# Kernel optimization log

Measured on AMD Instinct MI355X. Metric: run time of the kernel, lower is better.

The kernel has to match this reference:

```python
import jax, jax.numpy as jnp
import numpy as np

B, C, H, W = 4, 128, 256, 256
N_KPTS = 2048
N_POS = 8
KS = 3
CH = 2 * N_POS  # channel_num (mask=False)


def setup_inputs() -> dict:
    key = jax.random.key(0)
    ks = jax.random.split(key, 8)
    x = jax.random.normal(ks[0], (B, C, H, W), jnp.float32)
    keypoints = jax.random.uniform(ks[1], (B, N_KPTS, 2), jnp.float32, -1.0, 1.0)
    s1 = 1.0 / np.sqrt(C * KS * KS)
    W1 = jax.random.uniform(ks[2], (CH, C, KS, KS), jnp.float32, -s1, s1)
    b1 = jax.random.uniform(ks[3], (CH,), jnp.float32, -s1, s1)
    s2 = 1.0 / np.sqrt(CH)
    W2 = jax.random.uniform(ks[4], (CH, CH), jnp.float32, -s2, s2)
    b2 = jax.random.uniform(ks[5], (CH,), jnp.float32, -s2, s2)
    s3 = 1.0 / np.sqrt(C)
    sf_w = jax.random.uniform(ks[6], (C, C), jnp.float32, -s3, s3)
    agg_w = jax.random.uniform(ks[7], (N_POS, C, C), jnp.float32)  # torch.rand
    return {"x": x, "keypoints": keypoints, "W1": W1, "b1": b1,
            "W2": W2, "b2": b2, "sf_w": sf_w, "agg_w": agg_w}


def _bilinear(img, px, py):
    """grid_sample(bilinear, align_corners=True, padding=zeros) in pixel coords.
    img: [c,h,w]; px,py: [M] -> [c,M]."""
    h, w = img.shape[1], img.shape[2]
    x0f = jnp.floor(px); y0f = jnp.floor(py)
    x0 = x0f.astype(jnp.int32); y0 = y0f.astype(jnp.int32)
    wx1 = px - x0f; wy1 = py - y0f
    wx0 = 1.0 - wx1; wy0 = 1.0 - wy1

    def tap(yi, xi, wgt):
        valid = (xi >= 0) & (xi < w) & (yi >= 0) & (yi < h)
        v = img[:, jnp.clip(yi, 0, h - 1), jnp.clip(xi, 0, w - 1)]
        return v * (wgt * valid)[None]

    return (tap(y0, x0, wy0 * wx0) + tap(y0, x0 + 1, wy0 * wx1)
            + tap(y0 + 1, x0, wy1 * wx0) + tap(y0 + 1, x0 + 1, wy1 * wx1))


def reference(x, keypoints, W1, b1, W2, b2, sf_w, agg_w):
    wh = jnp.array([W - 1, H - 1], jnp.float32)
    max_off = max(H, W) / 4.0
    taps = jnp.arange(KS)

    def per_image(xi, kpts):
        kwh = (kpts / 2.0 + 0.5) * wh                     # [N,2] pixel coords (x,y)
        rc = kwh.astype(jnp.int32)                        # .long() trunc (coords >= 0)
        # corner = trunc(rc - ps/2 + 1) then clamp -> rc-1 clamped (ps=3)
        lim = jnp.array([W - 1 - KS, H - 1 - KS])
        corner = jnp.clip(rc - 1, 0, lim)                 # [N,2] (x,y)
        rows = corner[:, 1, None] + taps                  # [N,ks]
        cols = corner[:, 0, None] + taps                  # [N,ks]
        patch = xi[:, rows[:, :, None], cols[:, None, :]] # [c,N,ks,ks]
        patch = patch.transpose(1, 0, 2, 3)               # [N,c,ks,ks]
        # offset_conv: 3x3 conv (valid, ->1x1) + ReLU + 1x1 conv
        h1 = jax.nn.relu(jnp.einsum('ncab,ocab->no', patch, W1) + b1)
        off = h1 @ W2.T + b2                              # [N,2*n_pos]
        off = jnp.clip(off, -max_off, max_off)
        offset = off.reshape(-1, 2, N_POS).transpose(0, 2, 1)  # [N,n_pos,2]
        pos = kwh[:, None, :] + offset                    # [N,n_pos,2] pixel coords
        # 2*pos/wh - 1 then align_corners unnormalize == pos
        feat = _bilinear(xi, pos[..., 0].reshape(-1), pos[..., 1].reshape(-1))  # [c,N*p]
        feat = feat.reshape(C, -1, N_POS).transpose(1, 0, 2)  # [N,c,p]
        feat = jax.nn.selu(jnp.einsum('oc,ncp->nop', sf_w, feat))
        descs = jnp.einsum('ncp,pcd->nd', feat, agg_w)    # [N,dims]
        nrm = jnp.maximum(jnp.linalg.norm(descs, axis=1, keepdims=True), 1e-12)
        return descs / nrm, offset

    descriptors, offsets = jax.vmap(per_image)(x, keypoints)
    return descriptors, offsets
```

## Files before the change

kernel.cpp:

```cpp
#include <hip/hip_runtime.h>
#include <hip/hip_bf16.h>
#include <math.h>

#define B_ 4
#define C_ 128
#define H_ 256
#define W_ 256
#define NK 2048
#define NP 8
#define HW_ (H_*W_)
#define MAXOFF 64.0f
#define NROWS (B_*NK)

typedef short s16x8 __attribute__((ext_vector_type(8)));
typedef short s16x4 __attribute__((ext_vector_type(4)));
typedef float f32x4 __attribute__((ext_vector_type(4)));

#define SELU_SC 1.0507009873554805f
#define SELU_AL 1.6732632423543772f

#define N_W1F (36*64*8)
#define N_SFB (8*4*64*8)
#define N_AGG (8*8*4*64*8)

__device__ inline float bf2f(short b) {
    union { unsigned int u; float f; } cv;
    cv.u = ((unsigned int)(unsigned short)b) << 16;
    return cv.f;
}
__device__ inline short f2bf_s(float f) {
    __hip_bfloat16 h = __float2bfloat16(f);
    return *(short*)&h;
}

__global__ __launch_bounds__(256) void k_transpose_bf(const float* __restrict__ x,
                                                      __hip_bfloat16* __restrict__ xt) {
    __shared__ float tile[32][33];
    int bid = blockIdx.x;
    int xb = bid & 7;  bid >>= 3;
    int cb = bid & 3;  bid >>= 2;
    int y  = bid & 255; bid >>= 8;
    int i  = bid;
    int tx  = threadIdx.x & 31;
    int ty0 = threadIdx.x >> 5;
    const float* src = x + ((size_t)(i*C_ + cb*32)*H_ + y)*W_ + xb*32;
    #pragma unroll
    for (int k = 0; k < 4; ++k) {
        int c = ty0 + k*8;
        tile[c][tx] = src[(size_t)c*HW_ + tx];
    }
    __syncthreads();
    int tx2 = threadIdx.x & 15;
    int xo8 = threadIdx.x >> 4;
    __hip_bfloat16* dst = xt + ((size_t)(i*H_ + y)*W_ + xb*32)*C_ + cb*32;
    #pragma unroll
    for (int k = 0; k < 2; ++k) {
        int xo = xo8 + k*16;
        __hip_bfloat162 v;
        v.x = __float2bfloat16(tile[tx2*2][xo]);
        v.y = __float2bfloat16(tile[tx2*2+1][xo]);
        *(__hip_bfloat162*)(dst + (size_t)xo*C_ + tx2*2) = v;
    }
}

__global__ __launch_bounds__(256) void k_prep_all(const float* __restrict__ W1,
        const float* __restrict__ sf_w, const float* __restrict__ agg_w,
        __hip_bfloat16* __restrict__ w1f, __hip_bfloat16* __restrict__ sfb,
        __hip_bfloat16* __restrict__ aggb) {
    int t = blockIdx.x*256 + threadIdx.x;
    if (t < N_W1F) {
        int e = t & 7, l = (t >> 3) & 63, ks = t >> 9;
        int o = l & 15, c = (ks & 3)*32 + ((l >> 4) << 3) + e, ab = ks >> 2;
        w1f[t] = __float2bfloat16(W1[o*1152 + c*9 + ab]);
    } else if (t < N_W1F + N_SFB) {
        int u = t - N_W1F;
        int e = u & 7, l = (u >> 3) & 63, ks = (u >> 9) & 3, j = u >> 11;
        sfb[u] = __float2bfloat16(sf_w[(j*16 + (l & 15))*128 + ks*32 + ((l >> 4) << 3) + e]);
    } else if (t < N_W1F + N_SFB + N_AGG) {
        int u = t - N_W1F - N_SFB;
        int e = u & 7, l = (u >> 3) & 63, ks = (u >> 9) & 3, p = (u >> 11) & 7, jd = u >> 14;
        aggb[u] = __float2bfloat16(agg_w[((size_t)p*128 + ks*32 + ((l >> 4) << 3) + e)*128 + jd*16 + (l & 15)]);
    }
}

#define FSTR 1032
#define HSTR 136
#define RSTR 132
__global__ __launch_bounds__(256) void k_fused(
        const __hip_bfloat16* __restrict__ xtb, const float* __restrict__ kpts,
        const __hip_bfloat16* __restrict__ w1f, const float* __restrict__ b1,
        const float* __restrict__ W2, const float* __restrict__ b2,
        const __hip_bfloat16* __restrict__ sfb, const __hip_bfloat16* __restrict__ aggb,
        float* __restrict__ out_off, float* __restrict__ descs) {
    __shared__ __align__(16) char reg0[33792];
    __shared__ __align__(16) char reg1[17408];
    __shared__ float Cp[4][16][17];
    __shared__ float hL[16][17];
    __shared__ float W2s[16][16];
    __shared__ float posL[16][8][2];
    __shared__ float kwx[16], kwy[16];
    __shared__ int   kcx[16], kcy[16];

    int t = threadIdx.x;
    int blk = blockIdx.x;
    int i = blk >> 7;
    int w = t >> 6, l = t & 63;
    int r16 = l & 15, q = l >> 4;
    int kp0 = blk * 16;

    if (t < 16) {
        int gk = kp0 + t;
        float kx = kpts[(size_t)gk*2], ky = kpts[(size_t)gk*2 + 1];
        float wx = (kx*0.5f + 0.5f) * (float)(W_-1);
        float wy = (ky*0.5f + 0.5f) * (float)(H_-1);
        int cx = (int)wx - 1; cx = min(max(cx, 0), W_-1-3);
        int cy = (int)wy - 1; cy = min(max(cy, 0), H_-1-3);
        kwx[t] = wx; kwy[t] = wy; kcx[t] = cx; kcy[t] = cy;
    }
    W2s[t >> 4][t & 15] = W2[t];
    __syncthreads();

    {
        const char* pb = (const char*)(xtb +
            ((size_t)(i*H_ + kcy[r16])*W_ + kcx[r16])*C_);
        f32x4 acc = {0.f, 0.f, 0.f, 0.f};
        #pragma unroll
        for (int s = 0; s < 9; ++s) {
            int ks = w*9 + s;
            int ab = ks >> 2;
            int a = ab/3, b = ab - (ab/3)*3;
            int off = ((a*W_ + b)*C_ + (ks & 3)*32 + q*8) * 2;
            s16x8 af = *(const s16x8*)(pb + off);
            s16x8 bf = *(const s16x8*)((const short*)w1f + ((size_t)ks*64 + l)*8);
            acc = __builtin_amdgcn_mfma_f32_16x16x32_bf16(af, bf, acc, 0, 0, 0);
        }
        #pragma unroll
        for (int r = 0; r < 4; ++r)
            Cp[w][q*4 + r][r16] = acc[r];
    }
    __syncthreads();
    {
        int kp = t >> 4, o = t & 15;
        float sum = Cp[0][kp][o] + Cp[1][kp][o] + Cp[2][kp][o] + Cp[3][kp][o];
        hL[kp][o] = fmaxf(sum + b1[o], 0.f);
        __syncthreads();
        float acc2 = b2[o];
        #pragma unroll
        for (int oo = 0; oo < 16; ++oo)
            acc2 += hL[kp][oo] * W2s[o][oo];
        acc2 = fminf(fmaxf(acc2, -MAXOFF), MAXOFF);
        int d = o >> 3, p = o & 7;
        int gk = kp0 + kp;
        out_off[((size_t)gk*NP + p)*2 + d] = acc2;
        posL[kp][p][d] = (d ? kwy[kp] : kwx[kp]) + acc2;
    }
    __syncthreads();

    __hip_bfloat16* featL = (__hip_bfloat16*)reg0;
    {
        int half = t >> 5, lane32 = t & 31;
        int c0 = lane32 * 4;
        #pragma unroll 4
        for (int s = 0; s < 16; ++s) {
            int pr = s*8 + half;
            int kp = pr >> 3, p = pr & 7;
            float px = posL[kp][p][0], py = posL[kp][p][1];
            float x0f = floorf(px), y0f = floorf(py);
            int x0 = (int)x0f, y0 = (int)y0f;
            float wx1 = px - x0f, wy1 = py - y0f;
            float wx0 = 1.f - wx1, wy0 = 1.f - wy1;
            float a0 = 0.f, a1 = 0.f, a2 = 0.f, a3 = 0.f;
            #pragma unroll
            for (int tap = 0; tap < 4; ++tap) {
                int xi = x0 + (tap & 1);
                int yi = y0 + (tap >> 1);
                float wgt = ((tap & 1) ? wx1 : wx0) * ((tap >> 1) ? wy1 : wy0);
                bool valid = (xi >= 0) & (xi < W_) & (yi >= 0) & (yi < H_);
                int xc = min(max(xi, 0), W_-1);
                int yc = min(max(yi, 0), H_-1);
                float wv = valid ? wgt : 0.f;
                const __hip_bfloat16* src = xtb + ((size_t)(i*H_ + yc)*W_ + xc)*C_ + c0;
                s16x4 v = *(const s16x4*)src;
                a0 += wv * bf2f(v[0]);
                a1 += wv * bf2f(v[1]);
                a2 += wv * bf2f(v[2]);
                a3 += wv * bf2f(v[3]);
            }
            s16x4 ov;
            ov[0] = f2bf_s(a0); ov[1] = f2bf_s(a1);
            ov[2] = f2bf_s(a2); ov[3] = f2bf_s(a3);
            *(s16x4*)(featL + kp*FSTR + p*C_ + c0) = ov;
        }
    }
    __syncthreads();

    __hip_bfloat16* Hl = (__hip_bfloat16*)reg1;
    f32x4 dacc[8];
    #pragma unroll
    for (int jd = 0; jd < 8; ++jd) dacc[jd] = (f32x4){0.f,0.f,0.f,0.f};
    #pragma unroll
    for (int pi = 0; pi < 2; ++pi) {
        int p = w*2 + pi;
        s16x8 af[4];
        #pragma unroll
        for (int ks = 0; ks < 4; ++ks)
            af[ks] = *(const s16x8*)(featL + r16*FSTR + p*C_ + ks*32 + q*8);
        #pragma unroll
        for (int j = 0; j < 8; ++j) {
            f32x4 acc = (f32x4){0.f,0.f,0.f,0.f};
            const short* sb = (const short*)sfb + ((j*4)*64 + l)*8;
            #pragma unroll
            for (int ks = 0; ks < 4; ++ks)
                acc = __builtin_amdgcn_mfma_f32_16x16x32_bf16(af[ks], *(const s16x8*)(sb + ks*512), acc, 0, 0, 0);
            #pragma unroll
            for (int r = 0; r < 4; ++r) {
                float v = acc[r];
                v = v > 0.f ? SELU_SC*v : SELU_SC*SELU_AL*expm1f(v);
                Hl[(size_t)w*16*HSTR + (q*4 + r)*HSTR + j*16 + r16] = __float2bfloat16(v);
            }
        }
        s16x8 ah[4];
        #pragma unroll
        for (int ks = 0; ks < 4; ++ks)
            ah[ks] = *(const s16x8*)(Hl + (size_t)w*16*HSTR + r16*HSTR + ks*32 + q*8);
        #pragma unroll
        for (int jd = 0; jd < 8; ++jd) {
            const short* ab = (const short*)aggb + (((jd*8 + p)*4)*64 + l)*8;
            #pragma unroll
            for (int ks = 0; ks < 4; ++ks)
                dacc[jd] = __builtin_amdgcn_mfma_f32_16x16x32_bf16(ah[ks], *(const s16x8*)(ab + ks*512), dacc[jd], 0, 0, 0);
        }
    }
    __syncthreads();

    float* red = (float*)reg0;
    #pragma unroll
    for (int jd = 0; jd < 8; ++jd)
        #pragma unroll
        for (int r = 0; r < 4; ++r)
            red[((size_t)w*16 + q*4 + r)*RSTR + jd*16 + r16] = dacc[jd][r];
    __syncthreads();

    {
        int row = t >> 4, c0 = t & 15;
        float v[8];
        float ss = 0.f;
        #pragma unroll
        for (int k = 0; k < 8; ++k) {
            int col = c0 + 16*k;
            float s = red[(0*16 + row)*RSTR + col] + red[(1*16 + row)*RSTR + col]
                    + red[(2*16 + row)*RSTR + col] + red[(3*16 + row)*RSTR + col];
            v[k] = s; ss += s*s;
        }
        ss += __shfl_xor(ss, 1);
        ss += __shfl_xor(ss, 2);
        ss += __shfl_xor(ss, 4);
        ss += __shfl_xor(ss, 8);
        float sc = fmaxf(sqrtf(ss), 1e-12f);
        #pragma unroll
        for (int k = 0; k < 8; ++k)
            descs[(size_t)(kp0 + row)*C_ + c0 + 16*k] = v[k] / sc;
    }
}

__global__ __launch_bounds__(64) void k_offsets_f32(const float* __restrict__ xin,
        const float* __restrict__ kpts, const float* __restrict__ W1,
        const float* __restrict__ b1, const float* __restrict__ W2,
        const float* __restrict__ b2, float* __restrict__ out_off,
        float* __restrict__ pos) {
    __shared__ float pL[1152];
    __shared__ float hL2[16];
    __shared__ float oL[16];
    int bid = blockIdx.x;
    int i = bid >> 11;
    int t = threadIdx.x;
    float kx = kpts[(size_t)bid*2 + 0];
    float ky = kpts[(size_t)bid*2 + 1];
    float kwhx = (kx*0.5f + 0.5f) * (float)(W_-1);
    float kwhy = (ky*0.5f + 0.5f) * (float)(H_-1);
    int cx = (int)kwhx - 1; cx = cx < 0 ? 0 : (cx > 252 ? 252 : cx);
    int cy = (int)kwhy - 1; cy = cy < 0 ? 0 : (cy > 252 ? 252 : cy);
    for (int e = t; e < 1152; e += 64) {
        int a = e/384; int r = e - a*384; int b = r >> 7; int c = r & 127;
        pL[e] = xin[(((size_t)(i*C_ + c))*H_ + cy + a)*W_ + cx + b];
    }
    __syncthreads();
    int o = t & 15;
    int chunk = t >> 4;
    float partial = 0.f;
    const float* w1r = W1 + o*1152;
    for (int c = chunk*32; c < chunk*32 + 32; ++c) {
        #pragma unroll
        for (int ab = 0; ab < 9; ++ab) {
            const int a = ab/3, b = ab - (ab/3)*3;
            partial += w1r[c*9 + ab] * pL[a*384 + b*128 + c];
        }
    }
    partial += __shfl_xor(partial, 16);
    partial += __shfl_xor(partial, 32);
    float h1 = fmaxf(partial + b1[o], 0.f);
    if (t < 16) hL2[t] = h1;
    __syncthreads();
    if (t < 16) {
        float acc = b2[t];
        const float* w2r = W2 + t*16;
        #pragma unroll
        for (int oo = 0; oo < 16; ++oo) acc += w2r[oo]*hL2[oo];
        acc = fminf(fmaxf(acc, -MAXOFF), MAXOFF);
        oL[t] = acc;
    }
    __syncthreads();
    if (t < 8) {
        float ox = oL[t], oy = oL[8 + t];
        size_t base = ((size_t)bid*NP + t)*2;
        out_off[base]   = ox;
        out_off[base+1] = oy;
        pos[base]   = kwhx + ox;
        pos[base+1] = kwhy + oy;
    }
}

__global__ __launch_bounds__(128) void k_sample_f32(const float* __restrict__ xin,
        const float* __restrict__ pos, const float* __restrict__ sf_w,
        const float* __restrict__ agg_w, float* __restrict__ dst) {
    __shared__ __align__(16) float featL[NP*C_];
    __shared__ float pp[16];
    int bid = blockIdx.x;
    int i = bid >> 11;
    int c = threadIdx.x;
    if (c < 16) pp[c] = pos[(size_t)bid*16 + c];
    __syncthreads();
    #pragma unroll
    for (int p = 0; p < NP; ++p) {
        float px = pp[p*2], py = pp[p*2+1];
        float x0f = floorf(px), y0f = floorf(py);
        int x0 = (int)x0f, y0 = (int)y0f;
        float wx1 = px - x0f, wy1 = py - y0f;
        float wx0 = 1.f - wx1, wy0 = 1.f - wy1;
        float acc = 0.f;
        #pragma unroll
        for (int tap = 0; tap < 4; ++tap) {
            int xi = x0 + (tap & 1);
            int yi = y0 + (tap >> 1);
            float w = ((tap & 1) ? wx1 : wx0) * ((tap >> 1) ? wy1 : wy0);
            bool valid = (xi >= 0) & (xi < W_) & (yi >= 0) & (yi < H_);
            int xc = min(max(xi, 0), W_-1);
            int yc = min(max(yi, 0), H_-1);
            acc += (valid ? w : 0.f) * xin[(((size_t)(i*C_ + c))*H_ + yc)*W_ + xc];
        }
        featL[p*C_ + c] = acc;
    }
    __syncthreads();
    float acc[NP];
    #pragma unroll
    for (int p = 0; p < NP; ++p) acc[p] = 0.f;
    const float4* sfr = (const float4*)(sf_w + (size_t)c*C_);
    const float4* fL4 = (const float4*)featL;
    for (int c4 = 0; c4 < C_/4; ++c4) {
        float4 wv = sfr[c4];
        #pragma unroll
        for (int p = 0; p < NP; ++p) {
            float4 f = fL4[p*(C_/4) + c4];
            acc[p] += wv.x*f.x + wv.y*f.y + wv.z*f.z + wv.w*f.w;
        }
    }
    #pragma unroll
    for (int p = 0; p < NP; ++p) {
        float v = acc[p];
        acc[p] = v > 0.f ? SELU_SC*v : SELU_SC*SELU_AL*expm1f(v);
    }
    __shared__ __align__(16) float gL[NP*C_];
    #pragma unroll
    for (int p = 0; p < NP; ++p) gL[p*C_ + c] = acc[p];
    __syncthreads();
    float d_acc = 0.f;
    for (int pc = 0; pc < NP*C_; ++pc)
        d_acc += gL[pc] * agg_w[(size_t)pc*C_ + c];
    dst[(size_t)bid*C_ + c] = d_acc;
}

__global__ __launch_bounds__(64) void k_norm(float* __restrict__ out) {
    int row = blockIdx.x;
    int l = threadIdx.x;
    float* r = out + (size_t)row*C_;
    float a = r[l], b = r[l+64];
    float ss = a*a + b*b;
    #pragma unroll
    for (int m = 1; m < 64; m <<= 1) ss += __shfl_xor(ss, m);
    float s = fmaxf(sqrtf(ss), 1e-12f);
    r[l] = a/s; r[l+64] = b/s;
}

extern "C" void kernel_launch(void* const* d_in, const int* in_sizes, int n_in,
                              void* d_out, int out_size, void* d_ws, size_t ws_size,
                              hipStream_t stream) {
    const float* x    = (const float*)d_in[0];
    const float* kpts = (const float*)d_in[1];
    const float* W1   = (const float*)d_in[2];
    const float* b1   = (const float*)d_in[3];
    const float* W2   = (const float*)d_in[4];
    const float* b2   = (const float*)d_in[5];
    const float* sfw  = (const float*)d_in[6];
    const float* aggw = (const float*)d_in[7];
    float* out_desc = (float*)d_out;
    float* out_off  = out_desc + (size_t)B_*NK*C_;

    char* ws = (char*)d_ws;
    float* pos = (float*)ws;
    const size_t W1F_OFF = (size_t)1 << 20;
    const size_t SFB_OFF = (size_t)2 << 20;
    const size_t AGG_OFF = (size_t)3 << 20;
    const size_t XT_OFF  = (size_t)1 << 26;
    const size_t XT_BYTES = (size_t)B_*H_*W_*C_*2;
    bool useXT = ws_size >= XT_OFF + XT_BYTES;
    __hip_bfloat16* xtb  = (__hip_bfloat16*)(ws + XT_OFF);
    __hip_bfloat16* w1f  = (__hip_bfloat16*)(ws + W1F_OFF);
    __hip_bfloat16* sfb  = (__hip_bfloat16*)(ws + SFB_OFF);
    __hip_bfloat16* aggb = (__hip_bfloat16*)(ws + AGG_OFF);

    if (useXT) {
        const int NPREP = N_W1F + N_SFB + N_AGG;
        k_prep_all<<<(NPREP + 255)/256, 256, 0, stream>>>(W1, sfw, aggw, w1f, sfb, aggb);
        k_transpose_bf<<<B_*H_*(C_/32)*(W_/32), 256, 0, stream>>>(x, xtb);
        k_fused<<<NROWS/16, 256, 0, stream>>>(xtb, kpts, w1f, b1, W2, b2, sfb, aggb,
                                              out_off, out_desc);
    } else {
        k_offsets_f32<<<NROWS, 64, 0, stream>>>(x, kpts, W1, b1, W2, b2, out_off, pos);
        k_sample_f32<<<NROWS, 128, 0, stream>>>(x, pos, sfw, aggw, out_desc);
        k_norm<<<NROWS, 64, 0, stream>>>(out_desc);
    }
}
```

Baseline: 69.54 us.

## Merge weight prep into transpose kernel and shrink fused kernel LDS footprint

Result: faster. 66.83 us (-3.9%).

```diff
diff --git a/kernel.cpp b/kernel.cpp
--- a/kernel.cpp
+++ b/kernel.cpp
@@ -22,6 +22,9 @@
 #define N_W1F (36*64*8)
 #define N_SFB (8*4*64*8)
 #define N_AGG (8*8*4*64*8)
+#define NPREP (N_W1F + N_SFB + N_AGG)
+#define NT_BLK (B_*H_*(C_/32)*(W_/32))
+#define NP_BLK 81
 
 __device__ inline float bf2f(short b) {
     union { unsigned int u; float f; } cv;
@@ -33,10 +36,35 @@
     return *(short*)&h;
 }
 
-__global__ __launch_bounds__(256) void k_transpose_bf(const float* __restrict__ x,
-                                                      __hip_bfloat16* __restrict__ xt) {
+__global__ __launch_bounds__(256) void k_transpose_prep(const float* __restrict__ x,
+        __hip_bfloat16* __restrict__ xt,
+        const float* __restrict__ W1, const float* __restrict__ sf_w,
+        const float* __restrict__ agg_w,
+        __hip_bfloat16* __restrict__ w1f, __hip_bfloat16* __restrict__ sfb,
+        __hip_bfloat16* __restrict__ aggb) {
     __shared__ float tile[32][33];
     int bid = blockIdx.x;
+    if (bid >= NT_BLK) {
+        int base = ((bid - NT_BLK)*256 + threadIdx.x)*8;
+        #pragma unroll
+        for (int j = 0; j < 8; ++j) {
+            int t = base + j;
+            if (t < N_W1F) {
+                int e = t & 7, l = (t >> 3) & 63, ks = t >> 9;
+                int o = l & 15, c = (ks & 3)*32 + ((l >> 4) << 3) + e, ab = ks >> 2;
+                w1f[t] = __float2bfloat16(W1[o*1152 + c*9 + ab]);
+            } else if (t < N_W1F + N_SFB) {
+                int u = t - N_W1F;
+                int e = u & 7, l = (u >> 3) & 63, ks = (u >> 9) & 3, jj = u >> 11;
+                sfb[u] = __float2bfloat16(sf_w[(jj*16 + (l & 15))*128 + ks*32 + ((l >> 4) << 3) + e]);
+            } else if (t < NPREP) {
+                int u = t - N_W1F - N_SFB;
+                int e = u & 7, l = (u >> 3) & 63, ks = (u >> 9) & 3, p = (u >> 11) & 7, jd = u >> 14;
+                aggb[u] = __float2bfloat16(agg_w[((size_t)p*128 + ks*32 + ((l >> 4) << 3) + e)*128 + jd*16 + (l & 15)]);
+            }
+        }
+        return;
+    }
     int xb = bid & 7;  bid >>= 3;
     int cb = bid & 3;  bid >>= 2;
     int y  = bid & 255; bid >>= 8;
@@ -63,39 +91,16 @@
     }
 }
 
-__global__ __launch_bounds__(256) void k_prep_all(const float* __restrict__ W1,
-        const float* __restrict__ sf_w, const float* __restrict__ agg_w,
-        __hip_bfloat16* __restrict__ w1f, __hip_bfloat16* __restrict__ sfb,
-        __hip_bfloat16* __restrict__ aggb) {
-    int t = blockIdx.x*256 + threadIdx.x;
-    if (t < N_W1F) {
-        int e = t & 7, l = (t >> 3) & 63, ks = t >> 9;
-        int o = l & 15, c = (ks & 3)*32 + ((l >> 4) << 3) + e, ab = ks >> 2;
-        w1f[t] = __float2bfloat16(W1[o*1152 + c*9 + ab]);
-    } else if (t < N_W1F + N_SFB) {
-        int u = t - N_W1F;
-        int e = u & 7, l = (u >> 3) & 63, ks = (u >> 9) & 3, j = u >> 11;
-        sfb[u] = __float2bfloat16(sf_w[(j*16 + (l & 15))*128 + ks*32 + ((l >> 4) << 3) + e]);
-    } else if (t < N_W1F + N_SFB + N_AGG) {
-        int u = t - N_W1F - N_SFB;
-        int e = u & 7, l = (u >> 3) & 63, ks = (u >> 9) & 3, p = (u >> 11) & 7, jd = u >> 14;
-        aggb[u] = __float2bfloat16(agg_w[((size_t)p*128 + ks*32 + ((l >> 4) << 3) + e)*128 + jd*16 + (l & 15)]);
-    }
-}
-
 #define FSTR 1032
 #define HSTR 136
 #define RSTR 132
-__global__ __launch_bounds__(256) void k_fused(
+__global__ __launch_bounds__(256, 4) void k_fused(
         const __hip_bfloat16* __restrict__ xtb, const float* __restrict__ kpts,
         const __hip_bfloat16* __restrict__ w1f, const float* __restrict__ b1,
         const float* __restrict__ W2, const float* __restrict__ b2,
         const __hip_bfloat16* __restrict__ sfb, const __hip_bfloat16* __restrict__ aggb,
         float* __restrict__ out_off, float* __restrict__ descs) {
-    __shared__ __align__(16) char reg0[33792];
-    __shared__ __align__(16) char reg1[17408];
-    __shared__ float Cp[4][16][17];
-    __shared__ float hL[16][17];
+    __shared__ __align__(16) char smem[33792];
     __shared__ float W2s[16][16];
     __shared__ float posL[16][8][2];
     __shared__ float kwx[16], kwy[16];
@@ -120,6 +125,8 @@
     W2s[t >> 4][t & 15] = W2[t];
     __syncthreads();
 
+    float* Cp  = (float*)smem;
+    float* hLr = (float*)(smem + 4352);
     {
         const char* pb = (const char*)(xtb +
             ((size_t)(i*H_ + kcy[r16])*W_ + kcx[r16])*C_);
@@ -136,18 +143,19 @@
         }
         #pragma unroll
         for (int r = 0; r < 4; ++r)
-            Cp[w][q*4 + r][r16] = acc[r];
+            Cp[(w*16 + q*4 + r)*17 + r16] = acc[r];
     }
     __syncthreads();
     {
         int kp = t >> 4, o = t & 15;
-        float sum = Cp[0][kp][o] + Cp[1][kp][o] + Cp[2][kp][o] + Cp[3][kp][o];
-        hL[kp][o] = fmaxf(sum + b1[o], 0.f);
+        float sum = Cp[(0*16 + kp)*17 + o] + Cp[(1*16 + kp)*17 + o]
+                  + Cp[(2*16 + kp)*17 + o] + Cp[(3*16 + kp)*17 + o];
+        hLr[kp*17 + o] = fmaxf(sum + b1[o], 0.f);
         __syncthreads();
         float acc2 = b2[o];
         #pragma unroll
         for (int oo = 0; oo < 16; ++oo)
-            acc2 += hL[kp][oo] * W2s[o][oo];
+            acc2 += hLr[kp*17 + oo] * W2s[o][oo];
         acc2 = fminf(fmaxf(acc2, -MAXOFF), MAXOFF);
         int d = o >> 3, p = o & 7;
         int gk = kp0 + kp;
@@ -156,7 +164,7 @@
     }
     __syncthreads();
 
-    __hip_bfloat16* featL = (__hip_bfloat16*)reg0;
+    __hip_bfloat16* featL = (__hip_bfloat16*)smem;
     {
         int half = t >> 5, lane32 = t & 31;
         int c0 = lane32 * 4;
@@ -194,35 +202,41 @@
     }
     __syncthreads();
 
-    __hip_bfloat16* Hl = (__hip_bfloat16*)reg1;
-    f32x4 dacc[8];
-    #pragma unroll
-    for (int jd = 0; jd < 8; ++jd) dacc[jd] = (f32x4){0.f,0.f,0.f,0.f};
+    s16x8 af[2][4];
     #pragma unroll
     for (int pi = 0; pi < 2; ++pi) {
         int p = w*2 + pi;
-        s16x8 af[4];
         #pragma unroll
         for (int ks = 0; ks < 4; ++ks)
-            af[ks] = *(const s16x8*)(featL + r16*FSTR + p*C_ + ks*32 + q*8);
+            af[pi][ks] = *(const s16x8*)(featL + r16*FSTR + p*C_ + ks*32 + q*8);
+    }
+    __syncthreads();
+
+    __hip_bfloat16* Hl = (__hip_bfloat16*)(smem + (size_t)w*8448);
+    f32x4 dacc[8];
+    #pragma unroll
+    for (int jd = 0; jd < 8; ++jd) dacc[jd] = (f32x4){0.f,0.f,0.f,0.f};
+    #pragma unroll
+    for (int pi = 0; pi < 2; ++pi) {
+        int p = w*2 + pi;
         #pragma unroll
         for (int j = 0; j < 8; ++j) {
             f32x4 acc = (f32x4){0.f,0.f,0.f,0.f};
             const short* sb = (const short*)sfb + ((j*4)*64 + l)*8;
             #pragma unroll
             for (int ks = 0; ks < 4; ++ks)
-                acc = __builtin_amdgcn_mfma_f32_16x16x32_bf16(af[ks], *(const s16x8*)(sb + ks*512), acc, 0, 0, 0);
+                acc = __builtin_amdgcn_mfma_f32_16x16x32_bf16(af[pi][ks], *(const s16x8*)(sb + ks*512), acc, 0, 0, 0);
             #pragma unroll
             for (int r = 0; r < 4; ++r) {
                 float v = acc[r];
                 v = v > 0.f ? SELU_SC*v : SELU_SC*SELU_AL*expm1f(v);
-                Hl[(size_t)w*16*HSTR + (q*4 + r)*HSTR + j*16 + r16] = __float2bfloat16(v);
+                Hl[(q*4 + r)*HSTR + j*16 + r16] = __float2bfloat16(v);
             }
         }
         s16x8 ah[4];
         #pragma unroll
         for (int ks = 0; ks < 4; ++ks)
-            ah[ks] = *(const s16x8*)(Hl + (size_t)w*16*HSTR + r16*HSTR + ks*32 + q*8);
+            ah[ks] = *(const s16x8*)(Hl + r16*HSTR + ks*32 + q*8);
         #pragma unroll
         for (int jd = 0; jd < 8; ++jd) {
             const short* ab = (const short*)aggb + (((jd*8 + p)*4)*64 + l)*8;
@@ -233,7 +247,7 @@
     }
     __syncthreads();
 
-    float* red = (float*)reg0;
+    float* red = (float*)smem;
     #pragma unroll
     for (int jd = 0; jd < 8; ++jd)
         #pragma unroll
@@ -419,9 +433,8 @@
     __hip_bfloat16* aggb = (__hip_bfloat16*)(ws + AGG_OFF);
 
     if (useXT) {
-        const int NPREP = N_W1F + N_SFB + N_AGG;
-        k_prep_all<<<(NPREP + 255)/256, 256, 0, stream>>>(W1, sfw, aggw, w1f, sfb, aggb);
-        k_transpose_bf<<<B_*H_*(C_/32)*(W_/32), 256, 0, stream>>>(x, xtb);
+        k_transpose_prep<<<NT_BLK + NP_BLK, 256, 0, stream>>>(x, xtb, W1, sfw, aggw,
+                                                              w1f, sfb, aggb);
         k_fused<<<NROWS/16, 256, 0, stream>>>(xtb, kpts, w1f, b1, W2, b2, sfb, aggb,
                                               out_off, out_desc);
     } else {
```
